# Kernel tuning notes

Hardware: AMD Instinct MI355X
Metric: run time of the kernel (lower is better)

## Reference

```python
import jax, jax.numpy as jnp
import numpy as np

IGNORE_INDEX = 255


def setup_inputs() -> dict:
    key = jax.random.key(0)
    k1, k2, k3 = jax.random.split(key, 3)
    N, K, H, W = 8, 128, 256, 256
    out = jax.random.normal(k1, (N, K, H, W), dtype=jnp.float32)
    label = jax.random.uniform(k2, (N, 3, H, W), dtype=jnp.float32)
    centroids = jax.random.uniform(k3, (K, 3), dtype=jnp.float32)
    return {"out": out, "label": label, "centroids": centroids}


def reference(out, label, centroids):
    # out:   (N, K, H, W) logits over K clusters
    # label: (N, 3, H, W) continuous (e.g. color) targets
    # centroids: (K, 3)
    N, K, H, W = out.shape
    ignore_mask = jnp.any(label == float(IGNORE_INDEX), axis=1)  # (N, H, W)
    lab = jnp.transpose(label, (0, 2, 3, 1)).reshape(N, H * W, 3)  # (N, HW, 3)
    # squared Euclidean distance has the same argmin as cdist (p=2)
    d2 = (
        jnp.sum(lab * lab, axis=-1, keepdims=True)  # (N, HW, 1)
        - 2.0 * jnp.einsum("npc,kc->npk", lab, centroids)  # (N, HW, K)
        + jnp.sum(centroids * centroids, axis=-1)  # (K,)
    )
    idx = jnp.argmin(d2, axis=2).reshape(N, H, W)  # (N, H, W) int
    valid = ~ignore_mask  # (N, H, W)
    logp = jax.nn.log_softmax(out, axis=1)  # (N, K, H, W)
    picked = jnp.take_along_axis(logp, idx[:, None, :, :], axis=1)[:, 0]  # (N, H, W)
    num = -jnp.sum(jnp.where(valid, picked, 0.0))
    den = jnp.maximum(jnp.sum(valid.astype(jnp.float32)), 1.0)
    return num / den  # 'mean' reduction over non-ignored pixels
```

## Files before the change

kernel.cpp:

```cpp
#include <hip/hip_runtime.h>
#include <math.h>


constexpr int K_CL   = 128;
constexpr int NIMG   = 8;
constexpr int HW     = 256 * 256;
constexpr int BLOCK  = 256;
constexpr int TOTAL_PIX = NIMG * HW;
constexpr int NBLOCKS   = TOTAL_PIX / BLOCK;
constexpr float IGNORE_F = 255.0f;

__global__ __launch_bounds__(BLOCK) void cce_main(
    const float* __restrict__ logits,
    const float* __restrict__ label,
    const float* __restrict__ cent,
    float* __restrict__ partial_num,
    float* __restrict__ partial_cnt)
{
    __shared__ float sc[K_CL][4];
    const int t = threadIdx.x;
    if (t < K_CL) {
        float x = cent[t * 3 + 0];
        float y = cent[t * 3 + 1];
        float z = cent[t * 3 + 2];
        sc[t][0] = x; sc[t][1] = y; sc[t][2] = z;
        sc[t][3] = x * x + y * y + z * z;
    }
    __syncthreads();

    const int P = blockIdx.x * BLOCK + t;
    const int n = P >> 16;
    const int p = P & (HW - 1);

    const float* lb = label + ((long)n * 3) * HW + p;
    const float LX = lb[0];
    const float LY = lb[HW];
    const float LZ = lb[2 * HW];

    const float slab = LX * LX + LY * LY + LZ * LZ;
    float best = INFINITY;
    int   idx  = 0;
#pragma unroll 8
    for (int k = 0; k < K_CL; ++k) {
        float dot = LX * sc[k][0] + LY * sc[k][1] + LZ * sc[k][2];
        float d   = slab - 2.0f * dot + sc[k][3];
        if (d < best) { best = d; idx = k; }
    }

    const float* ob = logits + ((long)n * K_CL) * HW + p;
    float m = -INFINITY, s = 0.0f, vsel = 0.0f;
#pragma unroll 2
    for (int kb = 0; kb < K_CL; kb += 8) {
        float w[8];
#pragma unroll
        for (int u = 0; u < 8; ++u)
            w[u] = ob[(long)(kb + u) * HW];
#pragma unroll
        for (int u = 0; u < 8; ++u) {
            const int   k  = kb + u;
            const float vj = w[u];
            float e  = __expf(-fabsf(vj - m));
            bool  up = vj > m;
            s = up ? fmaf(s, e, 1.0f) : (s + e);
            m = fmaxf(m, vj);
            vsel = (k == idx) ? vj : vsel;
        }
    }

    const bool ignore = (LX == IGNORE_F) || (LY == IGNORE_F) || (LZ == IGNORE_F);
    float lsum = 0.0f, lcnt = 0.0f;
    if (!ignore) {
        lsum = vsel - m - __logf(s);
        lcnt = 1.0f;
    }

#pragma unroll
    for (int off = 32; off > 0; off >>= 1) {
        lsum += __shfl_down(lsum, off);
        lcnt += __shfl_down(lcnt, off);
    }
    __shared__ float wsum[BLOCK / 64], wcnt[BLOCK / 64];
    const int wave = t >> 6, lane = t & 63;
    if (lane == 0) { wsum[wave] = lsum; wcnt[wave] = lcnt; }
    __syncthreads();
    if (t == 0) {
        float a = 0.0f, c = 0.0f;
#pragma unroll
        for (int i = 0; i < BLOCK / 64; ++i) { a += wsum[i]; c += wcnt[i]; }
        partial_num[blockIdx.x] = a;
        partial_cnt[blockIdx.x] = c;
    }
}

__global__ __launch_bounds__(BLOCK) void cce_reduce(
    const float* __restrict__ partial_num,
    const float* __restrict__ partial_cnt,
    float* __restrict__ out,
    int nblocks)
{
    const int t = threadIdx.x;
    double s = 0.0, c = 0.0;
    for (int i = t; i < nblocks; i += BLOCK) {
        s += (double)partial_num[i];
        c += (double)partial_cnt[i];
    }
    __shared__ double sh_s[BLOCK], sh_c[BLOCK];
    sh_s[t] = s; sh_c[t] = c;
    __syncthreads();
    for (int off = BLOCK / 2; off > 0; off >>= 1) {
        if (t < off) { sh_s[t] += sh_s[t + off]; sh_c[t] += sh_c[t + off]; }
        __syncthreads();
    }
    if (t == 0) {
        double den = sh_c[0] > 1.0 ? sh_c[0] : 1.0;
        out[0] = (float)(-sh_s[0] / den);
    }
}

extern "C" void kernel_launch(void* const* d_in, const int* in_sizes, int n_in,
                              void* d_out, int out_size, void* d_ws, size_t ws_size,
                              hipStream_t stream)
{
    const float* logits = (const float*)d_in[0];
    const float* label  = (const float*)d_in[1];
    const float* cent   = (const float*)d_in[2];
    float* out = (float*)d_out;

    float* partial_num = (float*)d_ws;
    float* partial_cnt = partial_num + NBLOCKS;

    cce_main<<<NBLOCKS, BLOCK, 0, stream>>>(logits, label, cent, partial_num, partial_cnt);
    cce_reduce<<<1, BLOCK, 0, stream>>>(partial_num, partial_cnt, out, NBLOCKS);
}
```

Before: 54.98 us.

## Fuse final reduction via last-block atomic counter and use nontemporal loads

Replaces the separate single-block reduction kernel with a last-block-done pattern: each block atomically bumps a counter, and the final block sums all partials and writes the result. Logit and label reads become nontemporal loads and the logit prefetch batch widens from 8 to 16 values. This removes one kernel launch and its gap, at the cost of a memset per call, an atomic per block, and more registers for the wider batch.

```diff
diff --git a/kernel.cpp b/kernel.cpp
--- a/kernel.cpp
+++ b/kernel.cpp
@@ -10,12 +10,14 @@
 constexpr int NBLOCKS   = TOTAL_PIX / BLOCK;
 constexpr float IGNORE_F = 255.0f;
 
-__global__ __launch_bounds__(BLOCK) void cce_main(
+__global__ __launch_bounds__(BLOCK) void cce_fused(
     const float* __restrict__ logits,
     const float* __restrict__ label,
     const float* __restrict__ cent,
     float* __restrict__ partial_num,
-    float* __restrict__ partial_cnt)
+    float* __restrict__ partial_cnt,
+    int*   __restrict__ counter,
+    float* __restrict__ out)
 {
     __shared__ float sc[K_CL][4];
     const int t = threadIdx.x;
@@ -33,9 +35,9 @@
     const int p = P & (HW - 1);
 
     const float* lb = label + ((long)n * 3) * HW + p;
-    const float LX = lb[0];
-    const float LY = lb[HW];
-    const float LZ = lb[2 * HW];
+    const float LX = __builtin_nontemporal_load(lb);
+    const float LY = __builtin_nontemporal_load(lb + HW);
+    const float LZ = __builtin_nontemporal_load(lb + 2 * HW);
 
     const float slab = LX * LX + LY * LY + LZ * LZ;
     float best = INFINITY;
@@ -50,13 +52,13 @@
     const float* ob = logits + ((long)n * K_CL) * HW + p;
     float m = -INFINITY, s = 0.0f, vsel = 0.0f;
 #pragma unroll 2
-    for (int kb = 0; kb < K_CL; kb += 8) {
-        float w[8];
+    for (int kb = 0; kb < K_CL; kb += 16) {
+        float w[16];
 #pragma unroll
-        for (int u = 0; u < 8; ++u)
-            w[u] = ob[(long)(kb + u) * HW];
+        for (int u = 0; u < 16; ++u)
+            w[u] = __builtin_nontemporal_load(ob + (long)(kb + u) * HW);
 #pragma unroll
-        for (int u = 0; u < 8; ++u) {
+        for (int u = 0; u < 16; ++u) {
             const int   k  = kb + u;
             const float vj = w[u];
             float e  = __expf(-fabsf(vj - m));
@@ -83,37 +85,37 @@
     const int wave = t >> 6, lane = t & 63;
     if (lane == 0) { wsum[wave] = lsum; wcnt[wave] = lcnt; }
     __syncthreads();
+
+    __shared__ int sdone;
     if (t == 0) {
         float a = 0.0f, c = 0.0f;
 #pragma unroll
         for (int i = 0; i < BLOCK / 64; ++i) { a += wsum[i]; c += wcnt[i]; }
         partial_num[blockIdx.x] = a;
         partial_cnt[blockIdx.x] = c;
+        int prev = __hip_atomic_fetch_add(counter, 1, __ATOMIC_ACQ_REL,
+                                          __HIP_MEMORY_SCOPE_AGENT);
+        sdone = (prev == NBLOCKS - 1);
     }
-}
+    __syncthreads();
 
-__global__ __launch_bounds__(BLOCK) void cce_reduce(
-    const float* __restrict__ partial_num,
-    const float* __restrict__ partial_cnt,
-    float* __restrict__ out,
-    int nblocks)
-{
-    const int t = threadIdx.x;
-    double s = 0.0, c = 0.0;
-    for (int i = t; i < nblocks; i += BLOCK) {
-        s += (double)partial_num[i];
-        c += (double)partial_cnt[i];
-    }
-    __shared__ double sh_s[BLOCK], sh_c[BLOCK];
-    sh_s[t] = s; sh_c[t] = c;
-    __syncthreads();
-    for (int off = BLOCK / 2; off > 0; off >>= 1) {
-        if (t < off) { sh_s[t] += sh_s[t + off]; sh_c[t] += sh_c[t + off]; }
+    if (sdone) {
+        double rs = 0.0, rc = 0.0;
+        for (int i = t; i < NBLOCKS; i += BLOCK) {
+            rs += (double)partial_num[i];
+            rc += (double)partial_cnt[i];
+        }
+        __shared__ double sh_s[BLOCK], sh_c[BLOCK];
+        sh_s[t] = rs; sh_c[t] = rc;
         __syncthreads();
-    }
-    if (t == 0) {
-        double den = sh_c[0] > 1.0 ? sh_c[0] : 1.0;
-        out[0] = (float)(-sh_s[0] / den);
+        for (int off = BLOCK / 2; off > 0; off >>= 1) {
+            if (t < off) { sh_s[t] += sh_s[t + off]; sh_c[t] += sh_c[t + off]; }
+            __syncthreads();
+        }
+        if (t == 0) {
+            double den = sh_c[0] > 1.0 ? sh_c[0] : 1.0;
+            out[0] = (float)(-sh_s[0] / den);
+        }
     }
 }
 
@@ -128,7 +130,10 @@
 
     float* partial_num = (float*)d_ws;
     float* partial_cnt = partial_num + NBLOCKS;
+    int*   counter     = (int*)(partial_cnt + NBLOCKS);
 
-    cce_main<<<NBLOCKS, BLOCK, 0, stream>>>(logits, label, cent, partial_num, partial_cnt);
-    cce_reduce<<<1, BLOCK, 0, stream>>>(partial_num, partial_cnt, out, NBLOCKS);
+    hipMemsetAsync(counter, 0, sizeof(int), stream);
+    cce_fused<<<NBLOCKS, BLOCK, 0, stream>>>(logits, label, cent,
+                                             partial_num, partial_cnt,
+                                             counter, out);
 }
```

New measurement: 153.5 us. +179.2%, slower.
